# Optimization experiments

Measured on AMD Instinct MI355X. Metric: run time of the kernel, lower is better.

Reference implementation:

```python
import jax, jax.numpy as jnp
import numpy as np

EMBED = 1024
HEADS = 16
HEAD_DIM = EMBED // HEADS
EPS = 1e-6
T, S, B = 512, 512, 8


def setup_inputs() -> dict:
    key = jax.random.key(0)
    ks = jax.random.split(key, 8)
    ws = EMBED ** -0.5  # keep projected activations ~unit variance
    return {
        "q": jax.random.normal(ks[0], (T, B, EMBED), jnp.float32),
        "k": jax.random.normal(ks[1], (S, B, EMBED), jnp.float32),
        "v": jax.random.normal(ks[2], (S, B, EMBED), jnp.float32),
        "Wq": jax.random.normal(ks[3], (EMBED, EMBED), jnp.float32) * ws,
        "Wk": jax.random.normal(ks[4], (EMBED, EMBED), jnp.float32) * ws,
        "Wv": jax.random.normal(ks[5], (EMBED, EMBED), jnp.float32) * ws,
        "Wo": jax.random.normal(ks[6], (EMBED, EMBED), jnp.float32) * ws,
        "bo": jnp.zeros((EMBED,), jnp.float32),
        "energy_bias": jnp.full((1,), -2.0, jnp.float32),
    }


def _split_heads(x, L):
    # [L, B, E] -> [B*H, L, D]
    return x.reshape(L, B, HEADS, HEAD_DIM).transpose(1, 2, 0, 3).reshape(B * HEADS, L, HEAD_DIM)


def reference(q, k, v, Wq, Wk, Wv, Wo, bo, energy_bias):
    scaling = HEAD_DIM ** -0.5
    qp = _split_heads(jnp.einsum('tbe,ef->tbf', q, Wq) * scaling, T)  # [N,T,D]
    kp = _split_heads(jnp.einsum('sbe,ef->sbf', k, Wk), S)            # [N,S,D]
    vp = _split_heads(jnp.einsum('sbe,ef->sbf', v, Wv), S)            # [N,S,D]

    # monotonic energies + selection probabilities (deterministic, no noise)
    energy = jnp.einsum('ntd,nsd->nts', qp, kp) + energy_bias[0]       # [N,T,S]
    p_choose = jax.nn.sigmoid(energy)

    # exclusive cumprod of (1 - p) along src
    one_mp = 1.0 - p_choose
    shifted = jnp.concatenate([jnp.ones_like(one_mp[..., :1]), one_mp[..., :-1]], axis=-1)
    cumprod_1mp = jnp.cumprod(shifted, axis=-1)                        # [N,T,S]
    cumprod_clamp = jnp.clip(cumprod_1mp, EPS, 1.0)

    # alpha_i = clip(p_i * cumprod_i * cumsum(alpha_{i-1} / cumprod_clamp_i), 0, 1)
    N = B * HEADS
    init = jnp.zeros((N, S), p_choose.dtype).at[:, 0].set(1.0)

    def step(prev_alpha, xs):
        p_i, cp_i, cl_i = xs                                           # each [N,S]
        a = jnp.clip(p_i * cp_i * jnp.cumsum(prev_alpha / cl_i, axis=-1), 0.0, 1.0)
        return a, a

    xs = (p_choose.transpose(1, 0, 2), cumprod_1mp.transpose(1, 0, 2), cumprod_clamp.transpose(1, 0, 2))
    _, alpha = jax.lax.scan(step, init, xs)                            # [T,N,S]
    alpha = alpha.transpose(1, 0, 2)                                   # [N,T,S]

    # mass preservation: dump residual mass onto last source token
    alpha = alpha.at[..., -1].set(1.0 - jnp.clip(alpha[..., :-1].sum(axis=-1), 0.0, 1.0))

    beta = alpha  # hard monotonic attention: expected attention == alpha
    attn = jnp.einsum('nts,nsd->ntd', beta, vp)                        # [N,T,D]
    attn = attn.reshape(B, HEADS, T, HEAD_DIM).transpose(2, 0, 1, 3).reshape(T, B, EMBED)
    out = attn @ Wo + bo                                               # [T,B,E]
    return out
```

## Files before the change

### kernel.cpp

```cpp
#include <hip/hip_runtime.h>
#include <hip/hip_bf16.h>

#define T_DIM 512
#define S_DIM 512
#define B_DIM 8
#define E_DIM 1024
#define H_CNT 16
#define D_DIM 64
#define N_HEADS 128
#define M_ROWS 4096
#define K_DIM 1024
#define EPS_C 1e-6f

#define LDS_A   0
#define LDS_P   32768
#define LDS_X   65536
#define LDS_PCP 131072

using f32x4  = __attribute__((ext_vector_type(4))) float;
using short8 = __attribute__((ext_vector_type(8))) short;

static __device__ __forceinline__ ushort f2bf(float x){
  __hip_bfloat16 h = __float2bfloat16(x);
  return *reinterpret_cast<ushort*>(&h);
}
static __device__ __forceinline__ float bf2f_u(int u){
  return __int_as_float((u & 0xFFFF) << 16);
}
static __device__ __forceinline__ float rcpf(float x){
  return __builtin_amdgcn_rcpf(x);
}

template<int CTRL, int RMASK>
static __device__ __forceinline__ float dppf(float x, float oldv){
  return __int_as_float(__builtin_amdgcn_update_dpp(
      __float_as_int(oldv), __float_as_int(x), CTRL, RMASK, 0xf, false));
}
static __device__ __forceinline__ float wscan_mul(float x){
  x *= dppf<0x111,0xf>(x, 1.f);
  x *= dppf<0x112,0xf>(x, 1.f);
  x *= dppf<0x114,0xf>(x, 1.f);
  x *= dppf<0x118,0xf>(x, 1.f);
  x *= dppf<0x142,0xa>(x, 1.f);
  x *= dppf<0x143,0xc>(x, 1.f);
  return x;
}
static __device__ __forceinline__ float wscan_add(float x){
  x += dppf<0x111,0xf>(x, 0.f);
  x += dppf<0x112,0xf>(x, 0.f);
  x += dppf<0x114,0xf>(x, 0.f);
  x += dppf<0x118,0xf>(x, 0.f);
  x += dppf<0x142,0xa>(x, 0.f);
  x += dppf<0x143,0xc>(x, 0.f);
  return x;
}

__global__ __launch_bounds__(256) void wtrans4(const float* __restrict__ W0,
                                               const float* __restrict__ W1,
                                               const float* __restrict__ W2,
                                               const float* __restrict__ W3,
                                               ushort* __restrict__ T0,
                                               ushort* __restrict__ T1,
                                               ushort* __restrict__ T2,
                                               ushort* __restrict__ T3){
  const int z = blockIdx.z;
  const float* W = (z == 0) ? W0 : (z == 1) ? W1 : (z == 2) ? W2 : W3;
  ushort* Wt     = (z == 0) ? T0 : (z == 1) ? T1 : (z == 2) ? T2 : T3;
  __shared__ float tile[32][33];
  const int bx = blockIdx.x * 32, by = blockIdx.y * 32;
  const int x = threadIdx.x & 31, y = threadIdx.x >> 5;
  #pragma unroll
  for (int j = 0; j < 32; j += 8)
    tile[y + j][x] = W[(size_t)(by + y + j) * E_DIM + bx + x];
  __syncthreads();
  #pragma unroll
  for (int j = 0; j < 32; j += 8)
    Wt[(size_t)(bx + y + j) * E_DIM + by + x] = f2bf(tile[x][y + j]);
}

template<int MODE, bool ABF>
static __device__ __forceinline__ void gemm_core(const void* __restrict__ Ap,
                                                 const ushort* __restrict__ Bm,
                                                 void* __restrict__ Cout,
                                                 const float* __restrict__ bias,
                                                 int bx, int by){
  constexpr int BK = 32;
  __shared__ ushort lA[128 * BK];
  __shared__ ushort lB[128 * BK];
  const int tid = threadIdx.x;
  const int l = tid & 63, w = tid >> 6;
  const int wm = w >> 1, wn = w & 1;
  const int lq = l >> 4, lr = l & 15;
  const int m0 = by * 128, n0 = bx * 128;
  const int srow = tid >> 1, shalf = tid & 1;

  f32x4 acc[4][4];
  #pragma unroll
  for (int i = 0; i < 4; i++)
    #pragma unroll
    for (int j = 0; j < 4; j++) acc[i][j] = (f32x4){0.f, 0.f, 0.f, 0.f};

  for (int k0 = 0; k0 < K_DIM; k0 += BK){
    if constexpr (ABF){
      const ushort* ga = (const ushort*)Ap + (size_t)(m0 + srow) * K_DIM + k0 + shalf * 16;
      #pragma unroll
      for (int j = 0; j < 2; j++){
        short8 vv = *reinterpret_cast<const short8*>(ga + j * 8);
        int slot = (shalf * 2 + j) ^ (srow & 3);
        *reinterpret_cast<short8*>(reinterpret_cast<char*>(lA) + srow * 64 + slot * 16) = vv;
      }
    } else {
      const float* ga = (const float*)Ap + (size_t)(m0 + srow) * K_DIM + k0 + shalf * 16;
      ushort tmp[16];
      #pragma unroll
      for (int j = 0; j < 16; j += 4){
        float4 vv = *reinterpret_cast<const float4*>(ga + j);
        tmp[j] = f2bf(vv.x); tmp[j+1] = f2bf(vv.y); tmp[j+2] = f2bf(vv.z); tmp[j+3] = f2bf(vv.w);
      }
      #pragma unroll
      for (int j = 0; j < 2; j++){
        int slot = (shalf * 2 + j) ^ (srow & 3);
        *reinterpret_cast<short8*>(reinterpret_cast<char*>(lA) + srow * 64 + slot * 16) =
            *reinterpret_cast<short8*>(&tmp[j * 8]);
      }
    }
    {
      const ushort* gb = Bm + (size_t)(n0 + srow) * K_DIM + k0 + shalf * 16;
      #pragma unroll
      for (int j = 0; j < 2; j++){
        short8 vv = *reinterpret_cast<const short8*>(gb + j * 8);
        int slot = (shalf * 2 + j) ^ (srow & 3);
        *reinterpret_cast<short8*>(reinterpret_cast<char*>(lB) + srow * 64 + slot * 16) = vv;
      }
    }
    __syncthreads();
    short8 fa[4], fb[4];
    #pragma unroll
    for (int i = 0; i < 4; i++){
      int row = wm * 64 + i * 16 + lr;
      fa[i] = *reinterpret_cast<const short8*>(reinterpret_cast<const char*>(lA) + row * 64 + ((lq ^ (row & 3)) << 4));
      int col = wn * 64 + i * 16 + lr;
      fb[i] = *reinterpret_cast<const short8*>(reinterpret_cast<const char*>(lB) + col * 64 + ((lq ^ (col & 3)) << 4));
    }
    #pragma unroll
    for (int i = 0; i < 4; i++)
      #pragma unroll
      for (int j = 0; j < 4; j++)
        acc[i][j] = __builtin_amdgcn_mfma_f32_16x16x32_bf16(fa[i], fb[j], acc[i][j], 0, 0, 0);
    __syncthreads();
  }

  #pragma unroll
  for (int i = 0; i < 4; i++)
    #pragma unroll
    for (int j = 0; j < 4; j++)
      #pragma unroll
      for (int r = 0; r < 4; r++){
        int gm = m0 + wm * 64 + i * 16 + lq * 4 + r;
        int gn = n0 + wn * 64 + j * 16 + lr;
        float v = acc[i][j][r];
        if constexpr (MODE == 2){
          reinterpret_cast<float*>(Cout)[(size_t)gm * E_DIM + gn] = v + bias[gn];
        } else if constexpr (MODE == 3){
          int s = gm >> 3, b = gm & 7, h = gn >> 6, d = gn & 63;
          reinterpret_cast<ushort*>(Cout)[(((size_t)(b * H_CNT + h) * D_DIM + d) << 9) + s] = f2bf(v);
        } else {
          if constexpr (MODE == 1) v *= 0.125f;
          int t = gm >> 3, b = gm & 7, h = gn >> 6, d = gn & 63;
          reinterpret_cast<ushort*>(Cout)[(((size_t)(b * H_CNT + h) * T_DIM + t) << 6) + d] = f2bf(v);
        }
      }
}

__global__ __launch_bounds__(256) void gemm_qkv(const float* __restrict__ q,
                                                const float* __restrict__ k,
                                                const float* __restrict__ v,
                                                const ushort* __restrict__ wqt,
                                                const ushort* __restrict__ wkt,
                                                const ushort* __restrict__ wvt,
                                                ushort* __restrict__ qp,
                                                ushort* __restrict__ kp,
                                                ushort* __restrict__ vpT){
  if (blockIdx.z == 0)      gemm_core<1,false>(q, wqt, qp,  nullptr, blockIdx.x, blockIdx.y);
  else if (blockIdx.z == 1) gemm_core<0,false>(k, wkt, kp,  nullptr, blockIdx.x, blockIdx.y);
  else                      gemm_core<3,false>(v, wvt, vpT, nullptr, blockIdx.x, blockIdx.y);
}

__global__ __launch_bounds__(256) void gemm_out(const ushort* __restrict__ attn_bf,
                                                const ushort* __restrict__ wot,
                                                float* __restrict__ out,
                                                const float* __restrict__ bo){
  gemm_core<2,true>(attn_bf, wot, out, bo, blockIdx.x, blockIdx.y);
}

__global__ __launch_bounds__(512) void rec_kernel(const ushort* __restrict__ qp,
                                                  const ushort* __restrict__ kp,
                                                  const ushort* __restrict__ vpT,
                                                  ushort* __restrict__ attn_bf,
                                                  const float* __restrict__ ebias_p){
  extern __shared__ char smem[];
  const int tid = threadIdx.x;
  const int l = tid & 63, w = tid >> 6;
  const int kg = l >> 4, lr = l & 15;
  const int n = blockIdx.x;
  const int bb = n >> 4, hh = n & 15;
  const float ebias = ebias_p[0];

  const ushort* qph = qp + (size_t)n * (T_DIM * D_DIM);
  const ushort* kph = kp + (size_t)n * (S_DIM * D_DIM);

  float ap[8];
  #pragma unroll
  for (int j = 0; j < 8; j++) ap[j] = 0.f;
  if (l == 0) ap[0] = 1.f;

  for (int ph = 0; ph <= 34; ++ph){
    if (w == 0){
      const int c = ph - 2;
      if (c >= 0 && c < 32){
        const char* xb = smem + LDS_X   + ((c & 1) << 15);
        const char* cb = smem + LDS_PCP + ((c & 1) << 14);
        char*       ab = smem + LDS_A   + ((c & 1) << 14);
        f32x4 c0 = *reinterpret_cast<const f32x4*>(xb + (l << 5));
        f32x4 c1 = *reinterpret_cast<const f32x4*>(xb + (l << 5) + 16);
        short8 pv = *reinterpret_cast<const short8*>(cb + (l << 4));
        #pragma unroll
        for (int tt = 0; tt < 16; ++tt){
          f32x4 n0v, n1v; short8 npv;
          if (tt < 15){
            n0v = *reinterpret_cast<const f32x4*>(xb + ((tt + 1) << 11) + (l << 5));
            n1v = *reinterpret_cast<const f32x4*>(xb + ((tt + 1) << 11) + (l << 5) + 16);
            npv = *reinterpret_cast<const short8*>(cb + ((tt + 1) << 10) + (l << 4));
          }
          float z0 = ap[0]*c0[0], z1 = ap[1]*c0[1], z2 = ap[2]*c0[2], z3 = ap[3]*c0[3];
          float z4 = ap[4]*c1[0], z5 = ap[5]*c1[1], z6 = ap[6]*c1[2], z7 = ap[7]*c1[3];
          float a1 = z0+z1, a3 = z2+z3, a5 = z4+z5, a7 = z6+z7;
          float b3 = a1+a3, b7 = a5+a7, e6 = a5+z6;
          float d0 = z0, d1 = a1, d2 = a1+z2, d3 = b3;
          float d4 = b3+z4, d5 = b3+a5, d6 = b3+e6, d7 = b3+b7;
          float Ta = wscan_add(d7);
          float Ea = dppf<0x138,0xf>(Ta, 0.f);
          float al[8];
          al[0] = fminf(bf2f_u(pv[0]) * (Ea + d0), 1.f);
          al[1] = fminf(bf2f_u(pv[1]) * (Ea + d1), 1.f);
          al[2] = fminf(bf2f_u(pv[2]) * (Ea + d2), 1.f);
          al[3] = fminf(bf2f_u(pv[3]) * (Ea + d3), 1.f);
          al[4] = fminf(bf2f_u(pv[4]) * (Ea + d4), 1.f);
          al[5] = fminf(bf2f_u(pv[5]) * (Ea + d5), 1.f);
          al[6] = fminf(bf2f_u(pv[6]) * (Ea + d6), 1.f);
          al[7] = fminf(bf2f_u(pv[7]) * (Ea + d7), 1.f);
          float ls = ((al[0]+al[1])+(al[2]+al[3])) + ((al[4]+al[5])+(al[6]+al[7]));
          float St = wscan_add(ls);
          short8 ob;
          #pragma unroll
          for (int j = 0; j < 8; j++){ ob[j] = (short)f2bf(al[j]); ap[j] = al[j]; }
          if (l == 63){
            float fx = 1.f - fminf(fmaxf(St - al[7], 0.f), 1.f);
            ob[7] = (short)f2bf(fx);
          }
          *reinterpret_cast<short8*>(ab + ((((tt) << 10) + (l << 4)) ^ ((tt & 7) << 4))) = ob;
          if (tt < 15){ c0 = n0v; c1 = n1v; pv = npv; }
        }
      }
    } else if (w <= 4){
      const int c = ph - 3;
      if (c >= 0){
        const int dcol = ((w - 1) << 4) + lr;
        const ushort* vb = vpT + ((size_t)n * 64 + dcol) * 512;
        const char* ab = smem + LDS_A + ((c & 1) << 14);
        f32x4 ac = (f32x4){0.f, 0.f, 0.f, 0.f};
        #pragma unroll
        for (int kk = 0; kk < 16; ++kk){
          int sb = kk * 32 + kg * 8;
          short8 faA = *reinterpret_cast<const short8*>(ab + (((lr << 10) + (sb << 1)) ^ ((lr & 7) << 4)));
          short8 fbV = *reinterpret_cast<const short8*>(vb + sb);
          ac = __builtin_amdgcn_mfma_f32_16x16x32_bf16(faA, fbV, ac, 0, 0, 0);
        }
        const int t0 = c << 4;
        #pragma unroll
        for (int r = 0; r < 4; ++r){
          int tg = t0 + (kg << 2) + r;
          attn_bf[((size_t)tg * B_DIM + bb) * E_DIM + hh * 64 + dcol] = f2bf(ac[r]);
        }
      }
    } else {
      const int cx = ph - 1;
      if (cx >= 0 && cx < 32){
        const char* pb = smem + LDS_P   + ((cx & 1) << 14);
        char*       xb = smem + LDS_X   + ((cx & 1) << 15);
        char*       cb = smem + LDS_PCP + ((cx & 1) << 14);
        for (int tt = w - 5; tt < 16; tt += 3){
          short8 uv = *reinterpret_cast<const short8*>(pb + (tt << 10) + (l << 4));
          float om[8], p[8];
          #pragma unroll
          for (int j = 0; j < 8; j++){
            om[j] = (float)(((int)uv[j]) & 0xFFFF) * (1.f / 65535.f);
            p[j] = 1.f - om[j];
          }
          float a1 = om[0]*om[1], a3 = om[2]*om[3], a5 = om[4]*om[5], a7 = om[6]*om[7];
          float b3 = a1*a3, b7 = a5*a7, e6 = a5*om[6];
          float m[8];
          m[0] = om[0]; m[1] = a1; m[2] = a1*om[2]; m[3] = b3;
          m[4] = b3*om[4]; m[5] = b3*a5; m[6] = b3*e6; m[7] = b3*b7;
          float Tm = wscan_mul(m[7]);
          float Em = dppf<0x138,0xf>(Tm, 1.f);
          float cp[8];
          cp[0] = Em;
          #pragma unroll
          for (int j = 1; j < 8; j++) cp[j] = Em * m[j-1];
          float cr[8], pc[8];
          #pragma unroll
          for (int j = 0; j < 8; j++){
            cr[j] = rcpf(fmaxf(cp[j], EPS_C));
            pc[j] = p[j] * cp[j];
          }
          f32x4 w0 = (f32x4){cr[0], cr[1], cr[2], cr[3]};
          f32x4 w1 = (f32x4){cr[4], cr[5], cr[6], cr[7]};
          *reinterpret_cast<f32x4*>(xb + (tt << 11) + (l << 5)) = w0;
          *reinterpret_cast<f32x4*>(xb + (tt << 11) + (l << 5) + 16) = w1;
          short8 pcb;
          #pragma unroll
          for (int j = 0; j < 8; j++) pcb[j] = (short)f2bf(pc[j]);
          *reinterpret_cast<short8*>(cb + (tt << 10) + (l << 4)) = pcb;
        }
      }
      const int ce = ph;
      if (ce < 32){
        const int t0 = ce << 4;
        char* pb = smem + LDS_P + ((ce & 1) << 14);
        short8 fa0 = *reinterpret_cast<const short8*>(qph + (t0 + lr) * 64 + kg * 8);
        short8 fa1 = *reinterpret_cast<const short8*>(qph + (t0 + lr) * 64 + 32 + kg * 8);
        for (int tile = w - 5; tile < 32; tile += 3){
          int s0 = tile << 4;
          short8 fb0 = *reinterpret_cast<const short8*>(kph + (s0 + lr) * 64 + kg * 8);
          short8 fb1 = *reinterpret_cast<const short8*>(kph + (s0 + lr) * 64 + 32 + kg * 8);
          f32x4 e = (f32x4){0.f, 0.f, 0.f, 0.f};
          e = __builtin_amdgcn_mfma_f32_16x16x32_bf16(fa0, fb0, e, 0, 0, 0);
          e = __builtin_amdgcn_mfma_f32_16x16x32_bf16(fa1, fb1, e, 0, 0, 0);
          #pragma unroll
          for (int r = 0; r < 4; ++r){
            float om = rcpf(1.f + __expf(e[r] + ebias));
            uint u = (uint)(om * 65535.f + 0.5f);
            *reinterpret_cast<ushort*>(pb + (((kg << 2) + r) << 10) + ((s0 + lr) << 1)) = (ushort)u;
          }
        }
      }
    }
    __syncthreads();
  }
}

extern "C" void kernel_launch(void* const* d_in, const int* in_sizes, int n_in,
                              void* d_out, int out_size, void* d_ws, size_t ws_size,
                              hipStream_t stream){
  (void)in_sizes; (void)n_in; (void)out_size; (void)ws_size;
  const float* q  = (const float*)d_in[0];
  const float* k  = (const float*)d_in[1];
  const float* v  = (const float*)d_in[2];
  const float* Wq = (const float*)d_in[3];
  const float* Wk = (const float*)d_in[4];
  const float* Wv = (const float*)d_in[5];
  const float* Wo = (const float*)d_in[6];
  const float* bo = (const float*)d_in[7];
  const float* eb = (const float*)d_in[8];

  char* ws = (char*)d_ws;
  ushort* wqt  = (ushort*)(ws);
  ushort* wkt  = (ushort*)(ws + (1u << 21));
  ushort* wvt  = (ushort*)(ws + 2u * (1u << 21));
  ushort* wot  = (ushort*)(ws + 3u * (1u << 21));
  ushort* qp   = (ushort*)(ws + 4u * (1u << 21));
  ushort* kp   = (ushort*)(ws + 4u * (1u << 21) + (1u << 23));
  ushort* vpT  = (ushort*)(ws + 4u * (1u << 21) + 2u * (1u << 23));
  ushort* attn = (ushort*)(ws + 4u * (1u << 21) + 3u * (1u << 23));

  wtrans4<<<dim3(32, 32, 4), dim3(256), 0, stream>>>(Wq, Wk, Wv, Wo, wqt, wkt, wvt, wot);

  gemm_qkv<<<dim3(E_DIM / 128, M_ROWS / 128, 3), dim3(256), 0, stream>>>(
      q, k, v, wqt, wkt, wvt, qp, kp, vpT);

  hipFuncSetAttribute((const void*)rec_kernel,
                      hipFuncAttributeMaxDynamicSharedMemorySize, 163840);
  rec_kernel<<<dim3(N_HEADS), dim3(512), 163840, stream>>>(qp, kp, vpT, attn, eb);

  gemm_out<<<dim3(E_DIM / 128, M_ROWS / 128), dim3(256), 0, stream>>>(attn, wot, (float*)d_out, bo);
}
```

Before: 403.8 us.

## Rebalance warp roles, swizzle LDS buffers, and use packed bf16 conversions in scan

```diff
diff --git a/kernel.cpp b/kernel.cpp
--- a/kernel.cpp
+++ b/kernel.cpp
@@ -24,11 +24,13 @@
   __hip_bfloat16 h = __float2bfloat16(x);
   return *reinterpret_cast<ushort*>(&h);
 }
-static __device__ __forceinline__ float bf2f_u(int u){
-  return __int_as_float((u & 0xFFFF) << 16);
-}
 static __device__ __forceinline__ float rcpf(float x){
   return __builtin_amdgcn_rcpf(x);
+}
+static __device__ __forceinline__ uint cvt_pk_bf16(float lo, float hi){
+  uint r;
+  asm("v_cvt_pk_bf16_f32 %0, %1, %2" : "=v"(r) : "v"(lo), "v"(hi));
+  return r;
 }
 
 template<int CTRL, int RMASK>
@@ -214,6 +216,10 @@
   for (int j = 0; j < 8; j++) ap[j] = 0.f;
   if (l == 0) ap[0] = 1.f;
 
+  const int xoA = (((l << 1)     ^ ((l >> 2) & 7)) << 4);
+  const int xoB = ((((l << 1)|1) ^ ((l >> 2) & 7)) << 4);
+  const int po  = ((l ^ ((l >> 3) & 7)) << 4);
+
   for (int ph = 0; ph <= 34; ++ph){
     if (w == 0){
       const int c = ph - 2;
@@ -221,17 +227,21 @@
         const char* xb = smem + LDS_X   + ((c & 1) << 15);
         const char* cb = smem + LDS_PCP + ((c & 1) << 14);
         char*       ab = smem + LDS_A   + ((c & 1) << 14);
-        f32x4 c0 = *reinterpret_cast<const f32x4*>(xb + (l << 5));
-        f32x4 c1 = *reinterpret_cast<const f32x4*>(xb + (l << 5) + 16);
-        short8 pv = *reinterpret_cast<const short8*>(cb + (l << 4));
+        f32x4 c0 = *reinterpret_cast<const f32x4*>(xb + xoA);
+        f32x4 c1 = *reinterpret_cast<const f32x4*>(xb + xoB);
+        uint4 pv = *reinterpret_cast<const uint4*>(cb + po);
         #pragma unroll
         for (int tt = 0; tt < 16; ++tt){
-          f32x4 n0v, n1v; short8 npv;
+          f32x4 n0v, n1v; uint4 npv;
           if (tt < 15){
-            n0v = *reinterpret_cast<const f32x4*>(xb + ((tt + 1) << 11) + (l << 5));
-            n1v = *reinterpret_cast<const f32x4*>(xb + ((tt + 1) << 11) + (l << 5) + 16);
-            npv = *reinterpret_cast<const short8*>(cb + ((tt + 1) << 10) + (l << 4));
+            n0v = *reinterpret_cast<const f32x4*>(xb + ((tt + 1) << 11) + xoA);
+            n1v = *reinterpret_cast<const f32x4*>(xb + ((tt + 1) << 11) + xoB);
+            npv = *reinterpret_cast<const uint4*>(cb + ((tt + 1) << 10) + po);
           }
+          float pc0 = __int_as_float(pv.x << 16), pc1 = __int_as_float(pv.x & 0xffff0000u);
+          float pc2 = __int_as_float(pv.y << 16), pc3 = __int_as_float(pv.y & 0xffff0000u);
+          float pc4 = __int_as_float(pv.z << 16), pc5 = __int_as_float(pv.z & 0xffff0000u);
+          float pc6 = __int_as_float(pv.w << 16), pc7 = __int_as_float(pv.w & 0xffff0000u);
           float z0 = ap[0]*c0[0], z1 = ap[1]*c0[1], z2 = ap[2]*c0[2], z3 = ap[3]*c0[3];
           float z4 = ap[4]*c1[0], z5 = ap[5]*c1[1], z6 = ap[6]*c1[2], z7 = ap[7]*c1[3];
           float a1 = z0+z1, a3 = z2+z3, a5 = z4+z5, a7 = z6+z7;
@@ -240,56 +250,52 @@
           float d4 = b3+z4, d5 = b3+a5, d6 = b3+e6, d7 = b3+b7;
           float Ta = wscan_add(d7);
           float Ea = dppf<0x138,0xf>(Ta, 0.f);
-          float al[8];
-          al[0] = fminf(bf2f_u(pv[0]) * (Ea + d0), 1.f);
-          al[1] = fminf(bf2f_u(pv[1]) * (Ea + d1), 1.f);
-          al[2] = fminf(bf2f_u(pv[2]) * (Ea + d2), 1.f);
-          al[3] = fminf(bf2f_u(pv[3]) * (Ea + d3), 1.f);
-          al[4] = fminf(bf2f_u(pv[4]) * (Ea + d4), 1.f);
-          al[5] = fminf(bf2f_u(pv[5]) * (Ea + d5), 1.f);
-          al[6] = fminf(bf2f_u(pv[6]) * (Ea + d6), 1.f);
-          al[7] = fminf(bf2f_u(pv[7]) * (Ea + d7), 1.f);
-          float ls = ((al[0]+al[1])+(al[2]+al[3])) + ((al[4]+al[5])+(al[6]+al[7]));
+          float al0 = fminf(pc0*(Ea+d0), 1.f), al1 = fminf(pc1*(Ea+d1), 1.f);
+          float al2 = fminf(pc2*(Ea+d2), 1.f), al3 = fminf(pc3*(Ea+d3), 1.f);
+          float al4 = fminf(pc4*(Ea+d4), 1.f), al5 = fminf(pc5*(Ea+d5), 1.f);
+          float al6 = fminf(pc6*(Ea+d6), 1.f), al7 = fminf(pc7*(Ea+d7), 1.f);
+          float ls = ((al0+al1)+(al2+al3)) + ((al4+al5)+(al6+al7));
           float St = wscan_add(ls);
-          short8 ob;
+          float fx = 1.f - fminf(fmaxf(St - al7, 0.f), 1.f);
+          uint4 ob;
+          ob.x = cvt_pk_bf16(al0, al1);
+          ob.y = cvt_pk_bf16(al2, al3);
+          ob.z = cvt_pk_bf16(al4, al5);
+          ob.w = cvt_pk_bf16(al6, (l == 63) ? fx : al7);
+          *reinterpret_cast<uint4*>(ab + (((tt << 10) + (l << 4)) ^ ((tt & 7) << 4))) = ob;
+          ap[0]=al0; ap[1]=al1; ap[2]=al2; ap[3]=al3;
+          ap[4]=al4; ap[5]=al5; ap[6]=al6; ap[7]=al7;
+          if (tt < 15){ c0 = n0v; c1 = n1v; pv = npv; }
+        }
+      }
+    } else if (w >= 6){
+      const int ce = ph;
+      if (ce < 32){
+        const int t0 = ce << 4;
+        char* pb = smem + LDS_P + ((ce & 1) << 14);
+        short8 fa0 = *reinterpret_cast<const short8*>(qph + (t0 + lr) * 64 + kg * 8);
+        short8 fa1 = *reinterpret_cast<const short8*>(qph + (t0 + lr) * 64 + 32 + kg * 8);
+        for (int tile = w - 6; tile < 32; tile += 2){
+          int s0 = tile << 4;
+          short8 fb0 = *reinterpret_cast<const short8*>(kph + (s0 + lr) * 64 + kg * 8);
+          short8 fb1 = *reinterpret_cast<const short8*>(kph + (s0 + lr) * 64 + 32 + kg * 8);
+          f32x4 e = (f32x4){0.f, 0.f, 0.f, 0.f};
+          e = __builtin_amdgcn_mfma_f32_16x16x32_bf16(fa0, fb0, e, 0, 0, 0);
+          e = __builtin_amdgcn_mfma_f32_16x16x32_bf16(fa1, fb1, e, 0, 0, 0);
           #pragma unroll
-          for (int j = 0; j < 8; j++){ ob[j] = (short)f2bf(al[j]); ap[j] = al[j]; }
-          if (l == 63){
-            float fx = 1.f - fminf(fmaxf(St - al[7], 0.f), 1.f);
-            ob[7] = (short)f2bf(fx);
+          for (int r = 0; r < 4; ++r){
+            float om = rcpf(1.f + __expf(e[r] + ebias));
+            uint u = (uint)(om * 65535.f + 0.5f);
+            *reinterpret_cast<ushort*>(pb + (((kg << 2) + r) << 10) + ((s0 + lr) << 1)) = (ushort)u;
           }
-          *reinterpret_cast<short8*>(ab + ((((tt) << 10) + (l << 4)) ^ ((tt & 7) << 4))) = ob;
-          if (tt < 15){ c0 = n0v; c1 = n1v; pv = npv; }
-        }
-      }
-    } else if (w <= 4){
-      const int c = ph - 3;
-      if (c >= 0){
-        const int dcol = ((w - 1) << 4) + lr;
-        const ushort* vb = vpT + ((size_t)n * 64 + dcol) * 512;
-        const char* ab = smem + LDS_A + ((c & 1) << 14);
-        f32x4 ac = (f32x4){0.f, 0.f, 0.f, 0.f};
-        #pragma unroll
-        for (int kk = 0; kk < 16; ++kk){
-          int sb = kk * 32 + kg * 8;
-          short8 faA = *reinterpret_cast<const short8*>(ab + (((lr << 10) + (sb << 1)) ^ ((lr & 7) << 4)));
-          short8 fbV = *reinterpret_cast<const short8*>(vb + sb);
-          ac = __builtin_amdgcn_mfma_f32_16x16x32_bf16(faA, fbV, ac, 0, 0, 0);
-        }
-        const int t0 = c << 4;
-        #pragma unroll
-        for (int r = 0; r < 4; ++r){
-          int tg = t0 + (kg << 2) + r;
-          attn_bf[((size_t)tg * B_DIM + bb) * E_DIM + hh * 64 + dcol] = f2bf(ac[r]);
-        }
-      }
-    } else {
+        }
+      }
       const int cx = ph - 1;
       if (cx >= 0 && cx < 32){
         const char* pb = smem + LDS_P   + ((cx & 1) << 14);
         char*       xb = smem + LDS_X   + ((cx & 1) << 15);
         char*       cb = smem + LDS_PCP + ((cx & 1) << 14);
-        for (int tt = w - 5; tt < 16; tt += 3){
+        for (int tt = w - 6; tt < 16; tt += 2){
           short8 uv = *reinterpret_cast<const short8*>(pb + (tt << 10) + (l << 4));
           float om[8], p[8];
           #pragma unroll
@@ -314,35 +320,41 @@
             cr[j] = rcpf(fmaxf(cp[j], EPS_C));
             pc[j] = p[j] * cp[j];
           }
-          f32x4 w0 = (f32x4){cr[0], cr[1], cr[2], cr[3]};
-          f32x4 w1 = (f32x4){cr[4], cr[5], cr[6], cr[7]};
-          *reinterpret_cast<f32x4*>(xb + (tt << 11) + (l << 5)) = w0;
-          *reinterpret_cast<f32x4*>(xb + (tt << 11) + (l << 5) + 16) = w1;
-          short8 pcb;
-          #pragma unroll
-          for (int j = 0; j < 8; j++) pcb[j] = (short)f2bf(pc[j]);
-          *reinterpret_cast<short8*>(cb + (tt << 10) + (l << 4)) = pcb;
-        }
-      }
-      const int ce = ph;
-      if (ce < 32){
-        const int t0 = ce << 4;
-        char* pb = smem + LDS_P + ((ce & 1) << 14);
-        short8 fa0 = *reinterpret_cast<const short8*>(qph + (t0 + lr) * 64 + kg * 8);
-        short8 fa1 = *reinterpret_cast<const short8*>(qph + (t0 + lr) * 64 + 32 + kg * 8);
-        for (int tile = w - 5; tile < 32; tile += 3){
-          int s0 = tile << 4;
-          short8 fb0 = *reinterpret_cast<const short8*>(kph + (s0 + lr) * 64 + kg * 8);
-          short8 fb1 = *reinterpret_cast<const short8*>(kph + (s0 + lr) * 64 + 32 + kg * 8);
-          f32x4 e = (f32x4){0.f, 0.f, 0.f, 0.f};
-          e = __builtin_amdgcn_mfma_f32_16x16x32_bf16(fa0, fb0, e, 0, 0, 0);
-          e = __builtin_amdgcn_mfma_f32_16x16x32_bf16(fa1, fb1, e, 0, 0, 0);
-          #pragma unroll
-          for (int r = 0; r < 4; ++r){
-            float om = rcpf(1.f + __expf(e[r] + ebias));
-            uint u = (uint)(om * 65535.f + 0.5f);
-            *reinterpret_cast<ushort*>(pb + (((kg << 2) + r) << 10) + ((s0 + lr) << 1)) = (ushort)u;
-          }
+          *reinterpret_cast<f32x4*>(xb + (tt << 11) + xoA) = (f32x4){cr[0], cr[1], cr[2], cr[3]};
+          *reinterpret_cast<f32x4*>(xb + (tt << 11) + xoB) = (f32x4){cr[4], cr[5], cr[6], cr[7]};
+          uint4 pcb;
+          pcb.x = cvt_pk_bf16(pc[0], pc[1]);
+          pcb.y = cvt_pk_bf16(pc[2], pc[3]);
+          pcb.z = cvt_pk_bf16(pc[4], pc[5]);
+          pcb.w = cvt_pk_bf16(pc[6], pc[7]);
+          *reinterpret_cast<uint4*>(cb + (tt << 10) + po) = pcb;
+        }
+      }
+    } else if (w != 4){
+      const int c = ph - 3;
+      if (c >= 0){
+        const int widx = (w == 5) ? 3 : (w - 1);
+        const int dcol = (widx << 4) + lr;
+        const ushort* vb = vpT + ((size_t)n * 64 + dcol) * 512;
+        const char* ab = smem + LDS_A + ((c & 1) << 14);
+        f32x4 ac0 = (f32x4){0.f, 0.f, 0.f, 0.f};
+        f32x4 ac1 = (f32x4){0.f, 0.f, 0.f, 0.f};
+        #pragma unroll
+        for (int kk = 0; kk < 8; ++kk){
+          int sbA = (2*kk)   * 32 + kg * 8;
+          int sbB = (2*kk+1) * 32 + kg * 8;
+          short8 faA = *reinterpret_cast<const short8*>(ab + (((lr << 10) + (sbA << 1)) ^ ((lr & 7) << 4)));
+          short8 fbA = *reinterpret_cast<const short8*>(vb + sbA);
+          ac0 = __builtin_amdgcn_mfma_f32_16x16x32_bf16(faA, fbA, ac0, 0, 0, 0);
+          short8 faB = *reinterpret_cast<const short8*>(ab + (((lr << 10) + (sbB << 1)) ^ ((lr & 7) << 4)));
+          short8 fbB = *reinterpret_cast<const short8*>(vb + sbB);
+          ac1 = __builtin_amdgcn_mfma_f32_16x16x32_bf16(faB, fbB, ac1, 0, 0, 0);
+        }
+        const int t0 = c << 4;
+        #pragma unroll
+        for (int r = 0; r < 4; ++r){
+          int tg = t0 + (kg << 2) + r;
+          attn_bf[((size_t)tg * B_DIM + bb) * E_DIM + hh * 64 + dcol] = f2bf(ac0[r] + ac1[r]);
         }
       }
     }
```

New measurement: 486.7 us. 1.21x slower.
